# Kernel tuning notes

Measured on AMD Instinct MI355X. Metric: run time of the kernel, lower is better.

The kernel has to match this reference:

```python
import jax, jax.numpy as jnp
import numpy as np

NUM_HEADS = 2
HIDDEN_DIM = 128  # == node_dim
HEAD_DIM = 64     # node_dim // num_heads
NEG_SLOPE = 0.2
N_NODES = 25000
N_EDGES = 400000
NODE_DIM = 128
EDGE_DIM = 64


def setup_inputs() -> dict:
    key = jax.random.key(0)
    ks = jax.random.split(key, 16)
    s = 0.05
    return {
        "node_features": jax.random.normal(ks[0], (N_NODES, NODE_DIM), jnp.float32),
        "edge_features": jax.random.normal(ks[1], (N_EDGES, EDGE_DIM), jnp.float32),
        "edge_index": jax.random.randint(ks[2], (2, N_EDGES), 0, N_NODES, jnp.int32),
        "ni_W": jax.random.normal(ks[3], (NODE_DIM, NUM_HEADS * HIDDEN_DIM), jnp.float32) * s,
        "ni_b": jax.random.normal(ks[4], (NUM_HEADS * HIDDEN_DIM,), jnp.float32) * s,
        "nj_W": jax.random.normal(ks[5], (NODE_DIM, NUM_HEADS * HIDDEN_DIM), jnp.float32) * s,
        "nj_b": jax.random.normal(ks[6], (NUM_HEADS * HIDDEN_DIM,), jnp.float32) * s,
        "e_W": jax.random.normal(ks[7], (EDGE_DIM, NUM_HEADS * HIDDEN_DIM), jnp.float32) * s,
        "e_b": jax.random.normal(ks[8], (NUM_HEADS * HIDDEN_DIM,), jnp.float32) * s,
        "attn_proj": jax.random.normal(ks[9], (NUM_HEADS, HIDDEN_DIM), jnp.float32),
        "msg_W": jax.random.normal(ks[10], (NODE_DIM + EDGE_DIM, NODE_DIM), jnp.float32) * s,
        "msg_b": jax.random.normal(ks[11], (NODE_DIM,), jnp.float32) * s,
        "out_W": jax.random.normal(ks[12], (NODE_DIM, NODE_DIM), jnp.float32) * s,
        "out_b": jax.random.normal(ks[13], (NODE_DIM,), jnp.float32) * s,
    }


def _scatter_softmax(logits, seg, num_segments):
    # logits: [E, H], seg: [E] -> per-destination-node softmax over incident edges
    seg_max = jax.ops.segment_max(logits, seg, num_segments=num_segments)  # [N, H]
    ex = jnp.exp(logits - seg_max[seg])
    denom = jax.ops.segment_sum(ex, seg, num_segments=num_segments)  # [N, H]
    return ex / denom[seg]


def reference(node_features, edge_features, edge_index, ni_W, ni_b, nj_W, nj_b,
              e_W, e_b, attn_proj, msg_W, msg_b, out_W, out_b):
    n_nodes = node_features.shape[0]
    dst = edge_index[0]  # aggregation index (indices()[0])
    src = edge_index[1]
    ni = node_features[dst]  # [E, D]
    nj = node_features[src]  # [E, D]

    hidden = ni @ ni_W + ni_b + nj @ nj_W + nj_b + edge_features @ e_W + e_b  # [E, H*hid]
    hidden = jnp.where(hidden >= 0, hidden, NEG_SLOPE * hidden)  # LeakyReLU
    hidden = hidden.reshape(-1, NUM_HEADS, HIDDEN_DIM)

    attn_logits = jnp.einsum('ehd,hd->eh', hidden, attn_proj)  # [E, H]
    attn = _scatter_softmax(attn_logits, dst, n_nodes)  # [E, H]

    messages = jnp.concatenate((nj, edge_features), axis=-1) @ msg_W + msg_b  # [E, D]
    messages = messages.reshape(-1, NUM_HEADS, HEAD_DIM) * attn[:, :, None]
    agg = jax.ops.segment_sum(messages, dst, num_segments=n_nodes)  # [N, H, head]
    agg = agg.reshape(n_nodes, NUM_HEADS * HEAD_DIM)
    return agg @ out_W + out_b
```

## Files before the change

### kernel.cpp

```cpp
#include <hip/hip_runtime.h>

#define NEG 0.2f
typedef unsigned short u16;
typedef __bf16 bf8 __attribute__((ext_vector_type(8)));
typedef float f4 __attribute__((ext_vector_type(4)));
typedef u16 u16x8 __attribute__((ext_vector_type(8)));

#define OFF_PREM  0ull
#define SZ_PREM   (25000ull*128ull)
#define OFF_P16   (OFF_PREM + SZ_PREM)
#define SZ_P16    (25000ull*256ull)
#define OFF_BCAT  (OFF_P16 + SZ_P16)
#define SZ_BCAT   (128ull*640ull)
#define OFF_BTOT  (OFF_BCAT + SZ_BCAT)
#define SZ_BTOT   256ull
#define OFF_LOG   (OFF_BTOT + SZ_BTOT)
#define SZ_LOG    (2ull*400000ull)
#define OFF_MAX   (OFF_LOG + SZ_LOG)
#define SZ_MAX    (2ull*25000ull)
#define OFF_DEN   (OFF_MAX + SZ_MAX)
#define SZ_DEN    (2ull*25000ull)
#define OFF_AGG   (OFF_DEN + SZ_DEN)
#define SZ_AGG    (25000ull*128ull)
#define OFF_CNT   (OFF_AGG + SZ_AGG)
#define SZ_CNT    25000ull
#define OFF_CUR   (OFF_CNT + SZ_CNT)
#define SZ_CUR    25000ull
#define OFF_PERM  (OFF_CUR + SZ_CUR)
#define SZ_PERM   400000ull
#define OFF_DST   (OFF_PERM + SZ_PERM)
#define SZ_DST    400000ull
#define OFF_SRC   (OFF_DST + SZ_DST)
#define SZ_SRC    400000ull
#define OFF_EWF   (OFF_SRC + SZ_SRC)
#define SZ_EWF    8192ull
#define OFF_MWF   (OFF_EWF + SZ_EWF)
#define SZ_MWF    4096ull

__device__ __forceinline__ unsigned fkey(float f) {
    unsigned u = __float_as_uint(f);
    return (u & 0x80000000u) ? ~u : (u | 0x80000000u);
}
__device__ __forceinline__ float keyf(unsigned k) {
    unsigned u = (k & 0x80000000u) ? (k & 0x7fffffffu) : ~k;
    return __uint_as_float(u);
}
__device__ __forceinline__ u16 f2b(float f) {
    unsigned u = __float_as_uint(f);
    return (u16)((u + 0x7FFFu + ((u >> 16) & 1u)) >> 16);
}
__device__ __forceinline__ float b2f(u16 v) {
    return __uint_as_float(((unsigned)v) << 16);
}
__device__ __forceinline__ bf8 pack8(float4 a, float4 b) {
    union { u16 u[8]; bf8 v; } x;
    x.u[0] = f2b(a.x); x.u[1] = f2b(a.y); x.u[2] = f2b(a.z); x.u[3] = f2b(a.w);
    x.u[4] = f2b(b.x); x.u[5] = f2b(b.y); x.u[6] = f2b(b.z); x.u[7] = f2b(b.w);
    return x.v;
}

__global__ void k_prep(const float* __restrict__ niW, const float* __restrict__ njW,
                       const float* __restrict__ msgW, const float* __restrict__ eW,
                       const float* __restrict__ nib, const float* __restrict__ njb,
                       const float* __restrict__ eb,
                       float* __restrict__ bcat, float* __restrict__ btot,
                       u16* __restrict__ ewfrag, u16* __restrict__ msgfrag) {
    int idx = blockIdx.x * 256 + threadIdx.x;
    if (idx < 128 * 640) {
        int k = idx / 640, c = idx % 640;
        float v = (c < 256) ? niW[k * 256 + c]
                : (c < 512) ? njW[k * 256 + (c - 256)]
                            : msgW[k * 128 + (c - 512)];
        bcat[idx] = v;
    }
    if (idx < 16384) {
        int c = idx >> 10, s = (idx >> 9) & 1, ln = (idx >> 3) & 63, i = idx & 7;
        int k = s * 32 + ((ln >> 4) << 3) + i;
        int col = c * 16 + (ln & 15);
        ewfrag[idx] = f2b(eW[k * 256 + col]);
    }
    if (idx < 8192) {
        int c = idx >> 10, s = (idx >> 9) & 1, ln = (idx >> 3) & 63, i = idx & 7;
        int k = s * 32 + ((ln >> 4) << 3) + i;
        int col = c * 16 + (ln & 15);
        msgfrag[idx] = f2b(msgW[(128 + k) * 128 + col]);
    }
    if (blockIdx.x == 0 && threadIdx.x < 256) {
        int c = threadIdx.x;
        btot[c] = nib[c] + njb[c] + eb[c];
    }
}

__device__ __forceinline__ void gemm_tile(const float* Al, int astride, int acol0,
                                          const float* Bl, int trow, int tcol,
                                          float acc[4][8]) {
    for (int k4 = 0; k4 < 64; k4 += 4) {
        float ar[4][4];
#pragma unroll
        for (int r = 0; r < 4; ++r)
            *(float4*)ar[r] = *(const float4*)&Al[(trow * 4 + r) * astride + acol0 + k4];
#pragma unroll
        for (int kk = 0; kk < 4; ++kk) {
            float4 b0 = *(const float4*)&Bl[(k4 + kk) * 128 + tcol * 8];
            float4 b1 = *(const float4*)&Bl[(k4 + kk) * 128 + tcol * 8 + 4];
            float bv[8] = {b0.x, b0.y, b0.z, b0.w, b1.x, b1.y, b1.z, b1.w};
#pragma unroll
            for (int r = 0; r < 4; ++r) {
                float av = ar[r][kk];
#pragma unroll
                for (int j = 0; j < 8; ++j) acc[r][j] = fmaf(av, bv[j], acc[r][j]);
            }
        }
    }
}

__global__ __launch_bounds__(256) void k_node_pre(const float* __restrict__ nf,
                                                  const float* __restrict__ bcat,
                                                  u16* __restrict__ pre16,
                                                  float* __restrict__ premsg) {
    __shared__ float Al[64 * 128];
    __shared__ float Bl[64 * 128];
    int t = threadIdx.x, n0 = blockIdx.x * 64;
    int trow = t >> 4, tcol = t & 15;
#pragma unroll
    for (int q = 0; q < 8; ++q) {
        int g = t + 256 * q;
        int i = g >> 5, k4 = (g & 31) * 4;
        int n = n0 + i;
        float4 v = make_float4(0.f, 0.f, 0.f, 0.f);
        if (n < 25000) v = *(const float4*)&nf[(size_t)n * 128 + k4];
        *(float4*)&Al[i * 128 + k4] = v;
    }
    for (int cc = 0; cc < 5; ++cc) {
        float acc[4][8] = {};
        for (int kh = 0; kh < 2; ++kh) {
            __syncthreads();
#pragma unroll
            for (int q = 0; q < 8; ++q) {
                int g = t + 256 * q;
                int k = g >> 5, c4 = (g & 31) * 4;
                *(float4*)&Bl[k * 128 + c4] =
                    *(const float4*)&bcat[(kh * 64 + k) * 640 + cc * 128 + c4];
            }
            __syncthreads();
            gemm_tile(Al, 128, kh * 64, Bl, trow, tcol, acc);
        }
#pragma unroll
        for (int r = 0; r < 4; ++r) {
            int n = n0 + trow * 4 + r;
            if (n < 25000) {
                if (cc < 4) {
                    u16x8 h8;
#pragma unroll
                    for (int j = 0; j < 8; ++j) h8[j] = f2b(acc[r][j]);
                    *(u16x8*)&pre16[(size_t)n * 512 + cc * 128 + tcol * 8] = h8;
                } else {
                    *(float4*)&premsg[(size_t)n * 128 + tcol * 8] =
                        make_float4(acc[r][0], acc[r][1], acc[r][2], acc[r][3]);
                    *(float4*)&premsg[(size_t)n * 128 + tcol * 8 + 4] =
                        make_float4(acc[r][4], acc[r][5], acc[r][6], acc[r][7]);
                }
            }
        }
        __syncthreads();
    }
}

__global__ void k_hist(const int* __restrict__ eidx, int* __restrict__ count) {
    int e = blockIdx.x * 256 + threadIdx.x;
    if (e < 400000) atomicAdd(&count[eidx[e]], 1);
}

__global__ __launch_bounds__(1024) void k_scan(const int* __restrict__ count,
                                               int* __restrict__ cursor) {
    __shared__ int sums[1024];
    int t = threadIdx.x;
    int base = t * 25;
    int v[25];
    int local = 0;
#pragma unroll
    for (int i = 0; i < 25; ++i) {
        int idx = base + i;
        int c = (idx < 25000) ? count[idx] : 0;
        v[i] = local;
        local += c;
    }
    sums[t] = local;
    __syncthreads();
    for (int off = 1; off < 1024; off <<= 1) {
        int x = (t >= off) ? sums[t - off] : 0;
        __syncthreads();
        sums[t] += x;
        __syncthreads();
    }
    int prefix = (t == 0) ? 0 : sums[t - 1];
#pragma unroll
    for (int i = 0; i < 25; ++i) {
        int idx = base + i;
        if (idx < 25000) cursor[idx] = prefix + v[i];
    }
}

__global__ void k_scatter(const int* __restrict__ eidx, int* __restrict__ cursor,
                          int* __restrict__ perm, int* __restrict__ dsts,
                          int* __restrict__ srcs) {
    int e = blockIdx.x * 256 + threadIdx.x;
    if (e < 400000) {
        int d = eidx[e];
        int p = atomicAdd(&cursor[d], 1);
        perm[p] = e;
        dsts[p] = d;
        srcs[p] = eidx[400000 + e];
    }
}

__global__ __launch_bounds__(256) void k_edge_logits(
        const float* __restrict__ ef, const int* __restrict__ perm,
        const int* __restrict__ dsts, const int* __restrict__ srcs,
        const u16* __restrict__ ewfrag, const u16* __restrict__ pre16,
        const float* __restrict__ btot, const float* __restrict__ aproj,
        float* __restrict__ logits_s, unsigned* __restrict__ maxkey) {
    __shared__ int eperm[64], dstl[64], srcl[64];
    int t = threadIdx.x;
    int w = t >> 6, l = t & 63;
    int p0 = blockIdx.x * 64;
    int row = l & 15, kb = l >> 4;

    if (t < 64) {
        eperm[t] = perm[p0 + t];
        dstl[t] = dsts[p0 + t];
        srcl[t] = srcs[p0 + t];
    }
    __syncthreads();

    int ea = eperm[w * 16 + row];
    const float* ap = &ef[(size_t)ea * 64 + kb * 8];
    float4 a00 = *(const float4*)ap;
    float4 a01 = *(const float4*)(ap + 4);
    float4 a10 = *(const float4*)(ap + 32);
    float4 a11 = *(const float4*)(ap + 36);
    bf8 a0 = pack8(a00, a01), a1 = pack8(a10, a11);

    int ed[4], es[4];
#pragma unroll
    for (int r = 0; r < 4; ++r) {
        int i4 = w * 16 + kb * 4 + r;
        ed[r] = dstl[i4];
        es[r] = srcl[i4];
    }

    float part0[4] = {0.f, 0.f, 0.f, 0.f}, part1[4] = {0.f, 0.f, 0.f, 0.f};
#pragma unroll
    for (int c = 0; c < 16; ++c) {
        bf8 b0 = *(const bf8*)&ewfrag[(size_t)((c * 2 + 0) * 64 + l) * 8];
        bf8 b1 = *(const bf8*)&ewfrag[(size_t)((c * 2 + 1) * 64 + l) * 8];
        f4 acc = {0.f, 0.f, 0.f, 0.f};
        acc = __builtin_amdgcn_mfma_f32_16x16x32_bf16(a0, b0, acc, 0, 0, 0);
        acc = __builtin_amdgcn_mfma_f32_16x16x32_bf16(a1, b1, acc, 0, 0, 0);
        int col = c * 16 + row;
        float bt = btot[col], apj = aproj[col];
#pragma unroll
        for (int r = 0; r < 4; ++r) {
            float pi = b2f(pre16[(size_t)ed[r] * 512 + col]);
            float pj = b2f(pre16[(size_t)es[r] * 512 + 256 + col]);
            float hid = acc[r] + pi + pj + bt;
            hid = hid >= 0.f ? hid : NEG * hid;
            if (c < 8) part0[r] = fmaf(hid, apj, part0[r]);
            else       part1[r] = fmaf(hid, apj, part1[r]);
        }
    }
#pragma unroll
    for (int m = 1; m < 16; m <<= 1) {
#pragma unroll
        for (int r = 0; r < 4; ++r) {
            part0[r] += __shfl_xor(part0[r], m);
            part1[r] += __shfl_xor(part1[r], m);
        }
    }
    if (row == 0) {
#pragma unroll
        for (int r = 0; r < 4; ++r) {
            int p = p0 + w * 16 + kb * 4 + r;
            logits_s[(size_t)p * 2 + 0] = part0[r];
            logits_s[(size_t)p * 2 + 1] = part1[r];
            atomicMax(&maxkey[ed[r] * 2 + 0], fkey(part0[r]));
            atomicMax(&maxkey[ed[r] * 2 + 1], fkey(part1[r]));
        }
    }
}

__global__ void k_soft(const int* __restrict__ dsts, float* __restrict__ logits_s,
                       const unsigned* __restrict__ maxkey, float* __restrict__ denom) {
    int idx = blockIdx.x * 256 + threadIdx.x;
    if (idx >= 800000) return;
    int p = idx >> 1, h = idx & 1;
    int d = dsts[p];
    float m = keyf(maxkey[d * 2 + h]);
    float ex = __expf(logits_s[idx] - m);
    logits_s[idx] = ex;
    atomicAdd(&denom[d * 2 + h], ex);
}

__global__ __launch_bounds__(256) void k_messages(
        const float* __restrict__ ef, const int* __restrict__ perm,
        const int* __restrict__ dsts, const int* __restrict__ srcs,
        const u16* __restrict__ msgfrag, const float* __restrict__ premsg,
        const float* __restrict__ exs, const float* __restrict__ denom,
        float* __restrict__ agg) {
    __shared__ float Msg[64 * 132];
    __shared__ int dstl[64], srcl[64], eperm[64];
    __shared__ float attl[64][2];
    int t = threadIdx.x;
    int w = t >> 6, l = t & 63;
    int p0 = blockIdx.x * 64;
    int row = l & 15, kb = l >> 4;

    if (t < 64) {
        int p = p0 + t;
        eperm[t] = perm[p];
        int d = dsts[p];
        dstl[t] = d;
        srcl[t] = srcs[p];
        attl[t][0] = exs[(size_t)p * 2 + 0] / denom[d * 2 + 0];
        attl[t][1] = exs[(size_t)p * 2 + 1] / denom[d * 2 + 1];
    }
    __syncthreads();

    int ea = eperm[w * 16 + row];
    const float* apr = &ef[(size_t)ea * 64 + kb * 8];
    float4 a00 = *(const float4*)apr;
    float4 a01 = *(const float4*)(apr + 4);
    float4 a10 = *(const float4*)(apr + 32);
    float4 a11 = *(const float4*)(apr + 36);
    bf8 a0 = pack8(a00, a01), a1 = pack8(a10, a11);

    int esr[4];
    float at0[4], at1[4];
#pragma unroll
    for (int r = 0; r < 4; ++r) {
        int i4 = w * 16 + kb * 4 + r;
        esr[r] = srcl[i4];
        at0[r] = attl[i4][0];
        at1[r] = attl[i4][1];
    }

#pragma unroll
    for (int c = 0; c < 8; ++c) {
        bf8 b0 = *(const bf8*)&msgfrag[(size_t)((c * 2 + 0) * 64 + l) * 8];
        bf8 b1 = *(const bf8*)&msgfrag[(size_t)((c * 2 + 1) * 64 + l) * 8];
        f4 acc = {0.f, 0.f, 0.f, 0.f};
        acc = __builtin_amdgcn_mfma_f32_16x16x32_bf16(a0, b0, acc, 0, 0, 0);
        acc = __builtin_amdgcn_mfma_f32_16x16x32_bf16(a1, b1, acc, 0, 0, 0);
        int col = c * 16 + row;
#pragma unroll
        for (int r = 0; r < 4; ++r) {
            float m = acc[r] + premsg[(size_t)esr[r] * 128 + col];
            float wm = ((c < 4) ? at0[r] : at1[r]) * m;
            Msg[(w * 16 + kb * 4 + r) * 132 + col] = wm;
        }
    }
    __syncthreads();

    int c = t & 127, half = t >> 7;
    int r0 = half * 32, r1 = r0 + 32;
    int cur = dstl[r0];
    float sum = 0.f;
    for (int r = r0; r < r1; ++r) {
        int d = dstl[r];
        if (d != cur) {
            atomicAdd(&agg[(size_t)cur * 128 + c], sum);
            sum = 0.f;
            cur = d;
        }
        sum += Msg[r * 132 + c];
    }
    atomicAdd(&agg[(size_t)cur * 128 + c], sum);
}

__global__ __launch_bounds__(256) void k_out(
        const float* __restrict__ agg, const float* __restrict__ denom,
        const float* __restrict__ msgb, const float* __restrict__ outW,
        const float* __restrict__ outb, float* __restrict__ out) {
    __shared__ float Al[64 * 128];
    __shared__ float Bl[64 * 128];
    int t = threadIdx.x, n0 = blockIdx.x * 64;
    int trow = t >> 4, tcol = t & 15;
#pragma unroll
    for (int q = 0; q < 8; ++q) {
        int g = t + 256 * q;
        int i = g >> 5, k4 = (g & 31) * 4;
        int n = n0 + i;
        float4 v = make_float4(0.f, 0.f, 0.f, 0.f);
        if (n < 25000) {
            v = *(const float4*)&agg[(size_t)n * 128 + k4];
            if (denom[n * 2 + (k4 >> 6)] > 0.f) {
                float4 mb = *(const float4*)&msgb[k4];
                v.x += mb.x; v.y += mb.y; v.z += mb.z; v.w += mb.w;
            }
        }
        *(float4*)&Al[i * 128 + k4] = v;
    }
    float acc[4][8] = {};
    for (int kh = 0; kh < 2; ++kh) {
        __syncthreads();
#pragma unroll
        for (int q = 0; q < 8; ++q) {
            int g = t + 256 * q;
            int k = g >> 5, c4 = (g & 31) * 4;
            *(float4*)&Bl[k * 128 + c4] = *(const float4*)&outW[(kh * 64 + k) * 128 + c4];
        }
        __syncthreads();
        gemm_tile(Al, 128, kh * 64, Bl, trow, tcol, acc);
    }
    float ob[8];
    *(float4*)ob = *(const float4*)&outb[tcol * 8];
    *(float4*)(ob + 4) = *(const float4*)&outb[tcol * 8 + 4];
#pragma unroll
    for (int r = 0; r < 4; ++r) {
        int n = n0 + trow * 4 + r;
        if (n < 25000) {
            *(float4*)&out[(size_t)n * 128 + tcol * 8] =
                make_float4(acc[r][0] + ob[0], acc[r][1] + ob[1], acc[r][2] + ob[2], acc[r][3] + ob[3]);
            *(float4*)&out[(size_t)n * 128 + tcol * 8 + 4] =
                make_float4(acc[r][4] + ob[4], acc[r][5] + ob[5], acc[r][6] + ob[6], acc[r][7] + ob[7]);
        }
    }
}

extern "C" void kernel_launch(void* const* d_in, const int* in_sizes, int n_in,
                              void* d_out, int out_size, void* d_ws, size_t ws_size,
                              hipStream_t stream) {
    const float* nf    = (const float*)d_in[0];
    const float* ef    = (const float*)d_in[1];
    const int*   eidx  = (const int*)d_in[2];
    const float* niW   = (const float*)d_in[3];
    const float* nib   = (const float*)d_in[4];
    const float* njW   = (const float*)d_in[5];
    const float* njb   = (const float*)d_in[6];
    const float* eW    = (const float*)d_in[7];
    const float* eb    = (const float*)d_in[8];
    const float* aproj = (const float*)d_in[9];
    const float* msgW  = (const float*)d_in[10];
    const float* msgb  = (const float*)d_in[11];
    const float* outW  = (const float*)d_in[12];
    const float* outb  = (const float*)d_in[13];

    float* ws = (float*)d_ws;
    float* premsg    = ws + OFF_PREM;
    u16*   pre16     = (u16*)(ws + OFF_P16);
    float* bcat      = ws + OFF_BCAT;
    float* btot      = ws + OFF_BTOT;
    float* logits_s  = ws + OFF_LOG;
    unsigned* maxkey = (unsigned*)(ws + OFF_MAX);
    float* denom     = ws + OFF_DEN;
    float* agg       = ws + OFF_AGG;
    int*   count     = (int*)(ws + OFF_CNT);
    int*   cursor    = (int*)(ws + OFF_CUR);
    int*   perm      = (int*)(ws + OFF_PERM);
    int*   dsts      = (int*)(ws + OFF_DST);
    int*   srcs      = (int*)(ws + OFF_SRC);
    u16*   ewfrag    = (u16*)(ws + OFF_EWF);
    u16*   msgfrag   = (u16*)(ws + OFF_MWF);

    hipMemsetAsync(ws + OFF_MAX, 0, (size_t)(SZ_MAX + SZ_DEN + SZ_AGG + SZ_CNT) * 4, stream);

    k_prep<<<320, 256, 0, stream>>>(niW, njW, msgW, eW, nib, njb, eb, bcat, btot, ewfrag, msgfrag);
    k_node_pre<<<391, 256, 0, stream>>>(nf, bcat, pre16, premsg);
    k_hist<<<1563, 256, 0, stream>>>(eidx, count);
    k_scan<<<1, 1024, 0, stream>>>(count, cursor);
    k_scatter<<<1563, 256, 0, stream>>>(eidx, cursor, perm, dsts, srcs);
    k_edge_logits<<<6250, 256, 0, stream>>>(ef, perm, dsts, srcs, ewfrag, pre16, btot, aproj, logits_s, maxkey);
    k_soft<<<3125, 256, 0, stream>>>(dsts, logits_s, maxkey, denom);
    k_messages<<<6250, 256, 0, stream>>>(ef, perm, dsts, srcs, msgfrag, premsg, logits_s, denom, agg);
    k_out<<<391, 256, 0, stream>>>(agg, denom, msgb, outW, outb, (float*)d_out);
}
```

Measured before the change: 364.4 us.

## Aggregate raw edge features and premsg, fold edge message weights into output GEMM

Result: slower. 400.8 us (+10.0%).

```diff
diff --git a/kernel.cpp b/kernel.cpp
--- a/kernel.cpp
+++ b/kernel.cpp
@@ -20,9 +20,11 @@
 #define SZ_MAX    (2ull*25000ull)
 #define OFF_DEN   (OFF_MAX + SZ_MAX)
 #define SZ_DEN    (2ull*25000ull)
-#define OFF_AGG   (OFF_DEN + SZ_DEN)
-#define SZ_AGG    (25000ull*128ull)
-#define OFF_CNT   (OFF_AGG + SZ_AGG)
+#define OFF_AGE   (OFF_DEN + SZ_DEN)
+#define SZ_AGE    (25000ull*128ull)
+#define OFF_AGP   (OFF_AGE + SZ_AGE)
+#define SZ_AGP    (25000ull*128ull)
+#define OFF_CNT   (OFF_AGP + SZ_AGP)
 #define SZ_CNT    25000ull
 #define OFF_CUR   (OFF_CNT + SZ_CNT)
 #define SZ_CUR    25000ull
@@ -34,8 +36,10 @@
 #define SZ_SRC    400000ull
 #define OFF_EWF   (OFF_SRC + SZ_SRC)
 #define SZ_EWF    8192ull
-#define OFF_MWF   (OFF_EWF + SZ_EWF)
-#define SZ_MWF    4096ull
+#define OFF_M1    (OFF_EWF + SZ_EWF)
+#define SZ_M1     16384ull
+#define OFF_MBW   (OFF_M1 + SZ_M1)
+#define SZ_MBW    128ull
 
 __device__ __forceinline__ unsigned fkey(float f) {
     unsigned u = __float_as_uint(f);
@@ -62,9 +66,11 @@
 __global__ void k_prep(const float* __restrict__ niW, const float* __restrict__ njW,
                        const float* __restrict__ msgW, const float* __restrict__ eW,
                        const float* __restrict__ nib, const float* __restrict__ njb,
-                       const float* __restrict__ eb,
+                       const float* __restrict__ eb, const float* __restrict__ msgb,
+                       const float* __restrict__ outW,
                        float* __restrict__ bcat, float* __restrict__ btot,
-                       u16* __restrict__ ewfrag, u16* __restrict__ msgfrag) {
+                       u16* __restrict__ ewfrag, float* __restrict__ M1,
+                       float* __restrict__ mbW) {
     int idx = blockIdx.x * 256 + threadIdx.x;
     if (idx < 128 * 640) {
         int k = idx / 640, c = idx % 640;
@@ -79,11 +85,19 @@
         int col = c * 16 + (ln & 15);
         ewfrag[idx] = f2b(eW[k * 256 + col]);
     }
-    if (idx < 8192) {
-        int c = idx >> 10, s = (idx >> 9) & 1, ln = (idx >> 3) & 63, i = idx & 7;
-        int k = s * 32 + ((ln >> 4) << 3) + i;
-        int col = c * 16 + (ln & 15);
-        msgfrag[idx] = f2b(msgW[(128 + k) * 128 + col]);
+    if (idx < 16384) {
+        int r = idx >> 7, c = idx & 127;
+        int h = r >> 6, k = r & 63;
+        float s = 0.f;
+        for (int j = 0; j < 64; ++j)
+            s = fmaf(msgW[(size_t)(128 + k) * 128 + h * 64 + j],
+                     outW[(size_t)(h * 64 + j) * 128 + c], s);
+        M1[idx] = s;
+    }
+    if (idx < 128) {
+        float s = 0.f;
+        for (int m = 0; m < 128; ++m) s = fmaf(msgb[m], outW[(size_t)m * 128 + idx], s);
+        mbW[idx] = s;
     }
     if (blockIdx.x == 0 && threadIdx.x < 256) {
         int c = threadIdx.x;
@@ -301,128 +315,118 @@
     atomicAdd(&denom[d * 2 + h], ex);
 }
 
-__global__ __launch_bounds__(256) void k_messages(
+__global__ __launch_bounds__(256) void k_msgagg(
         const float* __restrict__ ef, const int* __restrict__ perm,
         const int* __restrict__ dsts, const int* __restrict__ srcs,
-        const u16* __restrict__ msgfrag, const float* __restrict__ premsg,
         const float* __restrict__ exs, const float* __restrict__ denom,
-        float* __restrict__ agg) {
-    __shared__ float Msg[64 * 132];
-    __shared__ int dstl[64], srcl[64], eperm[64];
-    __shared__ float attl[64][2];
-    int t = threadIdx.x;
-    int w = t >> 6, l = t & 63;
-    int p0 = blockIdx.x * 64;
-    int row = l & 15, kb = l >> 4;
+        const float* __restrict__ premsg,
+        float* __restrict__ aggE, float* __restrict__ aggP) {
+    __shared__ float efL[64 * 68];
+    __shared__ float pmL[64 * 132];
+    __shared__ float attL[64][2];
+    __shared__ int dstl[64], el[64], sl[64];
+    int t = threadIdx.x, p0 = blockIdx.x * 64;
 
     if (t < 64) {
         int p = p0 + t;
-        eperm[t] = perm[p];
         int d = dsts[p];
         dstl[t] = d;
-        srcl[t] = srcs[p];
-        attl[t][0] = exs[(size_t)p * 2 + 0] / denom[d * 2 + 0];
-        attl[t][1] = exs[(size_t)p * 2 + 1] / denom[d * 2 + 1];
+        el[t] = perm[p];
+        sl[t] = srcs[p];
+        attL[t][0] = exs[(size_t)p * 2 + 0] / denom[d * 2 + 0];
+        attL[t][1] = exs[(size_t)p * 2 + 1] / denom[d * 2 + 1];
     }
     __syncthreads();
-
-    int ea = eperm[w * 16 + row];
-    const float* apr = &ef[(size_t)ea * 64 + kb * 8];
-    float4 a00 = *(const float4*)apr;
-    float4 a01 = *(const float4*)(apr + 4);
-    float4 a10 = *(const float4*)(apr + 32);
-    float4 a11 = *(const float4*)(apr + 36);
-    bf8 a0 = pack8(a00, a01), a1 = pack8(a10, a11);
-
-    int esr[4];
-    float at0[4], at1[4];
-#pragma unroll
-    for (int r = 0; r < 4; ++r) {
-        int i4 = w * 16 + kb * 4 + r;
-        esr[r] = srcl[i4];
-        at0[r] = attl[i4][0];
-        at1[r] = attl[i4][1];
-    }
-
-#pragma unroll
-    for (int c = 0; c < 8; ++c) {
-        bf8 b0 = *(const bf8*)&msgfrag[(size_t)((c * 2 + 0) * 64 + l) * 8];
-        bf8 b1 = *(const bf8*)&msgfrag[(size_t)((c * 2 + 1) * 64 + l) * 8];
-        f4 acc = {0.f, 0.f, 0.f, 0.f};
-        acc = __builtin_amdgcn_mfma_f32_16x16x32_bf16(a0, b0, acc, 0, 0, 0);
-        acc = __builtin_amdgcn_mfma_f32_16x16x32_bf16(a1, b1, acc, 0, 0, 0);
-        int col = c * 16 + row;
-#pragma unroll
-        for (int r = 0; r < 4; ++r) {
-            float m = acc[r] + premsg[(size_t)esr[r] * 128 + col];
-            float wm = ((c < 4) ? at0[r] : at1[r]) * m;
-            Msg[(w * 16 + kb * 4 + r) * 132 + col] = wm;
-        }
+#pragma unroll
+    for (int q = 0; q < 4; ++q) {
+        int g = t + 256 * q;
+        int r = g >> 4, ch = g & 15;
+        *(float4*)&efL[r * 68 + ch * 4] = *(const float4*)&ef[(size_t)el[r] * 64 + ch * 4];
+    }
+#pragma unroll
+    for (int q = 0; q < 8; ++q) {
+        int g = t + 256 * q;
+        int r = g >> 5, ch = g & 31;
+        *(float4*)&pmL[r * 132 + ch * 4] = *(const float4*)&premsg[(size_t)sl[r] * 128 + ch * 4];
     }
     __syncthreads();
 
-    int c = t & 127, half = t >> 7;
-    int r0 = half * 32, r1 = r0 + 32;
-    int cur = dstl[r0];
+    bool isE = t < 128;
+    int cc = isE ? t : (t - 128);
+    int h = cc >> 6;
+    int k = cc & 63;
+    float* base = isE ? aggE : aggP;
+    int cur = dstl[0];
     float sum = 0.f;
-    for (int r = r0; r < r1; ++r) {
+    for (int r = 0; r < 64; ++r) {
         int d = dstl[r];
         if (d != cur) {
-            atomicAdd(&agg[(size_t)cur * 128 + c], sum);
+            atomicAdd(&base[(size_t)cur * 128 + cc], sum);
             sum = 0.f;
             cur = d;
         }
-        sum += Msg[r * 132 + c];
-    }
-    atomicAdd(&agg[(size_t)cur * 128 + c], sum);
+        float v = isE ? efL[r * 68 + k] : pmL[r * 132 + cc];
+        sum = fmaf(attL[r][h], v, sum);
+    }
+    atomicAdd(&base[(size_t)cur * 128 + cc], sum);
 }
 
 __global__ __launch_bounds__(256) void k_out(
-        const float* __restrict__ agg, const float* __restrict__ denom,
-        const float* __restrict__ msgb, const float* __restrict__ outW,
+        const float* __restrict__ aggE, const float* __restrict__ aggP,
+        const int* __restrict__ count, const float* __restrict__ M1,
+        const float* __restrict__ outW, const float* __restrict__ mbW,
         const float* __restrict__ outb, float* __restrict__ out) {
     __shared__ float Al[64 * 128];
     __shared__ float Bl[64 * 128];
     int t = threadIdx.x, n0 = blockIdx.x * 64;
     int trow = t >> 4, tcol = t & 15;
-#pragma unroll
-    for (int q = 0; q < 8; ++q) {
-        int g = t + 256 * q;
-        int i = g >> 5, k4 = (g & 31) * 4;
-        int n = n0 + i;
-        float4 v = make_float4(0.f, 0.f, 0.f, 0.f);
-        if (n < 25000) {
-            v = *(const float4*)&agg[(size_t)n * 128 + k4];
-            if (denom[n * 2 + (k4 >> 6)] > 0.f) {
-                float4 mb = *(const float4*)&msgb[k4];
-                v.x += mb.x; v.y += mb.y; v.z += mb.z; v.w += mb.w;
-            }
-        }
-        *(float4*)&Al[i * 128 + k4] = v;
-    }
     float acc[4][8] = {};
-    for (int kh = 0; kh < 2; ++kh) {
+    for (int src = 0; src < 2; ++src) {
+        const float* Amat = src == 0 ? aggE : aggP;
+        const float* Bmat = src == 0 ? M1 : outW;
         __syncthreads();
 #pragma unroll
         for (int q = 0; q < 8; ++q) {
             int g = t + 256 * q;
-            int k = g >> 5, c4 = (g & 31) * 4;
-            *(float4*)&Bl[k * 128 + c4] = *(const float4*)&outW[(kh * 64 + k) * 128 + c4];
-        }
-        __syncthreads();
-        gemm_tile(Al, 128, kh * 64, Bl, trow, tcol, acc);
-    }
-    float ob[8];
+            int i = g >> 5, k4 = (g & 31) * 4;
+            int n = n0 + i;
+            float4 v = make_float4(0.f, 0.f, 0.f, 0.f);
+            if (n < 25000) v = *(const float4*)&Amat[(size_t)n * 128 + k4];
+            *(float4*)&Al[i * 128 + k4] = v;
+        }
+        for (int kh = 0; kh < 2; ++kh) {
+            __syncthreads();
+#pragma unroll
+            for (int q = 0; q < 8; ++q) {
+                int g = t + 256 * q;
+                int k = g >> 5, c4 = (g & 31) * 4;
+                *(float4*)&Bl[k * 128 + c4] = *(const float4*)&Bmat[(kh * 64 + k) * 128 + c4];
+            }
+            __syncthreads();
+            gemm_tile(Al, 128, kh * 64, Bl, trow, tcol, acc);
+        }
+    }
+    float ob[8], mb[8];
     *(float4*)ob = *(const float4*)&outb[tcol * 8];
     *(float4*)(ob + 4) = *(const float4*)&outb[tcol * 8 + 4];
+    *(float4*)mb = *(const float4*)&mbW[tcol * 8];
+    *(float4*)(mb + 4) = *(const float4*)&mbW[tcol * 8 + 4];
 #pragma unroll
     for (int r = 0; r < 4; ++r) {
         int n = n0 + trow * 4 + r;
         if (n < 25000) {
-            *(float4*)&out[(size_t)n * 128 + tcol * 8] =
-                make_float4(acc[r][0] + ob[0], acc[r][1] + ob[1], acc[r][2] + ob[2], acc[r][3] + ob[3]);
-            *(float4*)&out[(size_t)n * 128 + tcol * 8 + 4] =
-                make_float4(acc[r][4] + ob[4], acc[r][5] + ob[5], acc[r][6] + ob[6], acc[r][7] + ob[7]);
+            float hs = (count[n] > 0) ? 1.f : 0.f;
+            float4 o0, o1;
+            o0.x = acc[r][0] + ob[0] + hs * mb[0];
+            o0.y = acc[r][1] + ob[1] + hs * mb[1];
+            o0.z = acc[r][2] + ob[2] + hs * mb[2];
+            o0.w = acc[r][3] + ob[3] + hs * mb[3];
+            o1.x = acc[r][4] + ob[4] + hs * mb[4];
+            o1.y = acc[r][5] + ob[5] + hs * mb[5];
+            o1.z = acc[r][6] + ob[6] + hs * mb[6];
+            o1.w = acc[r][7] + ob[7] + hs * mb[7];
+            *(float4*)&out[(size_t)n * 128 + tcol * 8] = o0;
+            *(float4*)&out[(size_t)n * 128 + tcol * 8 + 4] = o1;
         }
     }
 }
@@ -453,24 +457,30 @@
     float* logits_s  = ws + OFF_LOG;
     unsigned* maxkey = (unsigned*)(ws + OFF_MAX);
     float* denom     = ws + OFF_DEN;
-    float* agg       = ws + OFF_AGG;
+    float* aggE      = ws + OFF_AGE;
+    float* aggP      = ws + OFF_AGP;
     int*   count     = (int*)(ws + OFF_CNT);
     int*   cursor    = (int*)(ws + OFF_CUR);
     int*   perm      = (int*)(ws + OFF_PERM);
     int*   dsts      = (int*)(ws + OFF_DST);
     int*   srcs      = (int*)(ws + OFF_SRC);
     u16*   ewfrag    = (u16*)(ws + OFF_EWF);
-    u16*   msgfrag   = (u16*)(ws + OFF_MWF);
-
-    hipMemsetAsync(ws + OFF_MAX, 0, (size_t)(SZ_MAX + SZ_DEN + SZ_AGG + SZ_CNT) * 4, stream);
-
-    k_prep<<<320, 256, 0, stream>>>(niW, njW, msgW, eW, nib, njb, eb, bcat, btot, ewfrag, msgfrag);
+    float* M1        = ws + OFF_M1;
+    float* mbW       = ws + OFF_MBW;
+
+    hipMemsetAsync(ws + OFF_MAX, 0,
+                   (size_t)(SZ_MAX + SZ_DEN + SZ_AGE + SZ_AGP + SZ_CNT) * 4, stream);
+
+    k_prep<<<320, 256, 0, stream>>>(niW, njW, msgW, eW, nib, njb, eb, msgb, outW,
+                                    bcat, btot, ewfrag, M1, mbW);
     k_node_pre<<<391, 256, 0, stream>>>(nf, bcat, pre16, premsg);
     k_hist<<<1563, 256, 0, stream>>>(eidx, count);
     k_scan<<<1, 1024, 0, stream>>>(count, cursor);
     k_scatter<<<1563, 256, 0, stream>>>(eidx, cursor, perm, dsts, srcs);
-    k_edge_logits<<<6250, 256, 0, stream>>>(ef, perm, dsts, srcs, ewfrag, pre16, btot, aproj, logits_s, maxkey);
+    k_edge_logits<<<6250, 256, 0, stream>>>(ef, perm, dsts, srcs, ewfrag, pre16,
+                                            btot, aproj, logits_s, maxkey);
     k_soft<<<3125, 256, 0, stream>>>(dsts, logits_s, maxkey, denom);
-    k_messages<<<6250, 256, 0, stream>>>(ef, perm, dsts, srcs, msgfrag, premsg, logits_s, denom, agg);
-    k_out<<<391, 256, 0, stream>>>(agg, denom, msgb, outW, outb, (float*)d_out);
-}
+    k_msgagg<<<6250, 256, 0, stream>>>(ef, perm, dsts, srcs, logits_s, denom,
+                                       premsg, aggE, aggP);
+    k_out<<<391, 256, 0, stream>>>(aggE, aggP, count, M1, outW, mbW, outb, (float*)d_out);
+}
```

## Use bf16 MFMA for node pre-projection and store message pre-projection in bf16

Applied to the files above, without the earlier changes.

Result: faster. 324.3 us (-11.0%).

```diff
diff --git a/kernel.cpp b/kernel.cpp
--- a/kernel.cpp
+++ b/kernel.cpp
@@ -6,13 +6,13 @@
 typedef float f4 __attribute__((ext_vector_type(4)));
 typedef u16 u16x8 __attribute__((ext_vector_type(8)));
 
-#define OFF_PREM  0ull
-#define SZ_PREM   (25000ull*128ull)
-#define OFF_P16   (OFF_PREM + SZ_PREM)
+#define OFF_P16   0ull
 #define SZ_P16    (25000ull*256ull)
-#define OFF_BCAT  (OFF_P16 + SZ_P16)
-#define SZ_BCAT   (128ull*640ull)
-#define OFF_BTOT  (OFF_BCAT + SZ_BCAT)
+#define OFF_PM16  (OFF_P16 + SZ_P16)
+#define SZ_PM16   (25000ull*64ull)
+#define OFF_BCF   (OFF_PM16 + SZ_PM16)
+#define SZ_BCF    40960ull
+#define OFF_BTOT  (OFF_BCF + SZ_BCF)
 #define SZ_BTOT   256ull
 #define OFF_LOG   (OFF_BTOT + SZ_BTOT)
 #define SZ_LOG    (2ull*400000ull)
@@ -63,15 +63,19 @@
                        const float* __restrict__ msgW, const float* __restrict__ eW,
                        const float* __restrict__ nib, const float* __restrict__ njb,
                        const float* __restrict__ eb,
-                       float* __restrict__ bcat, float* __restrict__ btot,
+                       u16* __restrict__ bcf, float* __restrict__ btot,
                        u16* __restrict__ ewfrag, u16* __restrict__ msgfrag) {
     int idx = blockIdx.x * 256 + threadIdx.x;
-    if (idx < 128 * 640) {
-        int k = idx / 640, c = idx % 640;
-        float v = (c < 256) ? niW[k * 256 + c]
-                : (c < 512) ? njW[k * 256 + (c - 256)]
-                            : msgW[k * 128 + (c - 512)];
-        bcat[idx] = v;
+    if (idx < 81920) {
+        int fi = idx >> 9;
+        int ln = (idx >> 3) & 63, i = idx & 7;
+        int cb = fi >> 2, s = fi & 3;
+        int k = s * 32 + ((ln >> 4) << 3) + i;
+        int col = cb * 16 + (ln & 15);
+        float v = (col < 256) ? niW[k * 256 + col]
+                : (col < 512) ? njW[k * 256 + (col - 256)]
+                              : msgW[k * 128 + (col - 512)];
+        bcf[idx] = f2b(v);
     }
     if (idx < 16384) {
         int c = idx >> 10, s = (idx >> 9) & 1, ln = (idx >> 3) & 63, i = idx & 7;
@@ -85,10 +89,7 @@
         int col = c * 16 + (ln & 15);
         msgfrag[idx] = f2b(msgW[(128 + k) * 128 + col]);
     }
-    if (blockIdx.x == 0 && threadIdx.x < 256) {
-        int c = threadIdx.x;
-        btot[c] = nib[c] + njb[c] + eb[c];
-    }
+    if (idx < 256) btot[idx] = nib[idx] + njb[idx] + eb[idx];
 }
 
 __device__ __forceinline__ void gemm_tile(const float* Al, int astride, int acol0,
@@ -115,54 +116,39 @@
 }
 
 __global__ __launch_bounds__(256) void k_node_pre(const float* __restrict__ nf,
-                                                  const float* __restrict__ bcat,
+                                                  const u16* __restrict__ bcf,
                                                   u16* __restrict__ pre16,
-                                                  float* __restrict__ premsg) {
-    __shared__ float Al[64 * 128];
-    __shared__ float Bl[64 * 128];
-    int t = threadIdx.x, n0 = blockIdx.x * 64;
-    int trow = t >> 4, tcol = t & 15;
-#pragma unroll
-    for (int q = 0; q < 8; ++q) {
-        int g = t + 256 * q;
-        int i = g >> 5, k4 = (g & 31) * 4;
-        int n = n0 + i;
-        float4 v = make_float4(0.f, 0.f, 0.f, 0.f);
-        if (n < 25000) v = *(const float4*)&nf[(size_t)n * 128 + k4];
-        *(float4*)&Al[i * 128 + k4] = v;
-    }
-    for (int cc = 0; cc < 5; ++cc) {
-        float acc[4][8] = {};
-        for (int kh = 0; kh < 2; ++kh) {
-            __syncthreads();
-#pragma unroll
-            for (int q = 0; q < 8; ++q) {
-                int g = t + 256 * q;
-                int k = g >> 5, c4 = (g & 31) * 4;
-                *(float4*)&Bl[k * 128 + c4] =
-                    *(const float4*)&bcat[(kh * 64 + k) * 640 + cc * 128 + c4];
+                                                  u16* __restrict__ premsg16) {
+    int t = threadIdx.x, w = t >> 6, l = t & 63;
+    int n0 = blockIdx.x * 64 + w * 16;
+    int rsel = l & 15, kb = l >> 4;
+    int nA = n0 + rsel;
+    size_t nAc = (nA < 25000) ? (size_t)nA : 24999;
+    const float* ap = &nf[nAc * 128 + kb * 8];
+    bf8 a[4];
+#pragma unroll
+    for (int s = 0; s < 4; ++s) {
+        float4 x = *(const float4*)&ap[s * 32];
+        float4 y = *(const float4*)&ap[s * 32 + 4];
+        a[s] = pack8(x, y);
+    }
+    int nC = n0 + kb * 4;
+#pragma unroll 4
+    for (int cb = 0; cb < 40; ++cb) {
+        f4 acc = {0.f, 0.f, 0.f, 0.f};
+#pragma unroll
+        for (int s = 0; s < 4; ++s) {
+            bf8 b = *(const bf8*)&bcf[(size_t)((cb * 4 + s) * 64 + l) * 8];
+            acc = __builtin_amdgcn_mfma_f32_16x16x32_bf16(a[s], b, acc, 0, 0, 0);
+        }
+#pragma unroll
+        for (int r = 0; r < 4; ++r) {
+            int nn = nC + r;
+            if (nn < 25000) {
+                if (cb < 32) pre16[(size_t)nn * 512 + cb * 16 + rsel] = f2b(acc[r]);
+                else premsg16[(size_t)nn * 128 + (cb - 32) * 16 + rsel] = f2b(acc[r]);
             }
-            __syncthreads();
-            gemm_tile(Al, 128, kh * 64, Bl, trow, tcol, acc);
-        }
-#pragma unroll
-        for (int r = 0; r < 4; ++r) {
-            int n = n0 + trow * 4 + r;
-            if (n < 25000) {
-                if (cc < 4) {
-                    u16x8 h8;
-#pragma unroll
-                    for (int j = 0; j < 8; ++j) h8[j] = f2b(acc[r][j]);
-                    *(u16x8*)&pre16[(size_t)n * 512 + cc * 128 + tcol * 8] = h8;
-                } else {
-                    *(float4*)&premsg[(size_t)n * 128 + tcol * 8] =
-                        make_float4(acc[r][0], acc[r][1], acc[r][2], acc[r][3]);
-                    *(float4*)&premsg[(size_t)n * 128 + tcol * 8 + 4] =
-                        make_float4(acc[r][4], acc[r][5], acc[r][6], acc[r][7]);
-                }
-            }
-        }
-        __syncthreads();
+        }
     }
 }
 
@@ -304,7 +290,7 @@
 __global__ __launch_bounds__(256) void k_messages(
         const float* __restrict__ ef, const int* __restrict__ perm,
         const int* __restrict__ dsts, const int* __restrict__ srcs,
-        const u16* __restrict__ msgfrag, const float* __restrict__ premsg,
+        const u16* __restrict__ msgfrag, const u16* __restrict__ premsg16,
         const float* __restrict__ exs, const float* __restrict__ denom,
         float* __restrict__ agg) {
     __shared__ float Msg[64 * 132];
@@ -354,7 +340,7 @@
         int col = c * 16 + row;
 #pragma unroll
         for (int r = 0; r < 4; ++r) {
-            float m = acc[r] + premsg[(size_t)esr[r] * 128 + col];
+            float m = acc[r] + b2f(premsg16[(size_t)esr[r] * 128 + col]);
             float wm = ((c < 4) ? at0[r] : at1[r]) * m;
             Msg[(w * 16 + kb * 4 + r) * 132 + col] = wm;
         }
@@ -378,7 +364,7 @@
 }
 
 __global__ __launch_bounds__(256) void k_out(
-        const float* __restrict__ agg, const float* __restrict__ denom,
+        const float* __restrict__ agg, const int* __restrict__ count,
         const float* __restrict__ msgb, const float* __restrict__ outW,
         const float* __restrict__ outb, float* __restrict__ out) {
     __shared__ float Al[64 * 128];
@@ -393,7 +379,7 @@
         float4 v = make_float4(0.f, 0.f, 0.f, 0.f);
         if (n < 25000) {
             v = *(const float4*)&agg[(size_t)n * 128 + k4];
-            if (denom[n * 2 + (k4 >> 6)] > 0.f) {
+            if (count[n] > 0) {
                 float4 mb = *(const float4*)&msgb[k4];
                 v.x += mb.x; v.y += mb.y; v.z += mb.z; v.w += mb.w;
             }
@@ -446,9 +432,9 @@
     const float* outb  = (const float*)d_in[13];
 
     float* ws = (float*)d_ws;
-    float* premsg    = ws + OFF_PREM;
     u16*   pre16     = (u16*)(ws + OFF_P16);
-    float* bcat      = ws + OFF_BCAT;
+    u16*   premsg16  = (u16*)(ws + OFF_PM16);
+    u16*   bcf       = (u16*)(ws + OFF_BCF);
     float* btot      = ws + OFF_BTOT;
     float* logits_s  = ws + OFF_LOG;
     unsigned* maxkey = (unsigned*)(ws + OFF_MAX);
@@ -464,13 +450,16 @@
 
     hipMemsetAsync(ws + OFF_MAX, 0, (size_t)(SZ_MAX + SZ_DEN + SZ_AGG + SZ_CNT) * 4, stream);
 
-    k_prep<<<320, 256, 0, stream>>>(niW, njW, msgW, eW, nib, njb, eb, bcat, btot, ewfrag, msgfrag);
-    k_node_pre<<<391, 256, 0, stream>>>(nf, bcat, pre16, premsg);
+    k_prep<<<320, 256, 0, stream>>>(niW, njW, msgW, eW, nib, njb, eb,
+                                    bcf, btot, ewfrag, msgfrag);
+    k_node_pre<<<391, 256, 0, stream>>>(nf, bcf, pre16, premsg16);
     k_hist<<<1563, 256, 0, stream>>>(eidx, count);
     k_scan<<<1, 1024, 0, stream>>>(count, cursor);
     k_scatter<<<1563, 256, 0, stream>>>(eidx, cursor, perm, dsts, srcs);
-    k_edge_logits<<<6250, 256, 0, stream>>>(ef, perm, dsts, srcs, ewfrag, pre16, btot, aproj, logits_s, maxkey);
+    k_edge_logits<<<6250, 256, 0, stream>>>(ef, perm, dsts, srcs, ewfrag, pre16,
+                                            btot, aproj, logits_s, maxkey);
     k_soft<<<3125, 256, 0, stream>>>(dsts, logits_s, maxkey, denom);
-    k_messages<<<6250, 256, 0, stream>>>(ef, perm, dsts, srcs, msgfrag, premsg, logits_s, denom, agg);
-    k_out<<<391, 256, 0, stream>>>(agg, denom, msgb, outW, outb, (float*)d_out);
-}
+    k_messages<<<6250, 256, 0, stream>>>(ef, perm, dsts, srcs, msgfrag, premsg16,
+                                         logits_s, denom, agg);
+    k_out<<<391, 256, 0, stream>>>(agg, count, msgb, outW, outb, (float*)d_out);
+}
```
